# Kernel tuning notes

Measured on AMD Instinct MI355X. Metric: run time of the kernel, lower is better.

Reference implementation:

```python
import jax, jax.numpy as jnp
import numpy as np

B, N, F_IN, F_OUT = 1024, 92, 1024, 512
ALPHA = 0.2
NEG_INF = -9e15


def setup_inputs() -> dict:
    key = jax.random.key(0)
    k1, k2, k3, k4, k5, k6 = jax.random.split(key, 6)
    stdv = 1.0 / np.sqrt(F_OUT)
    inputs = {
        "input": jax.random.normal(k1, (B, N, F_IN), dtype=jnp.float32),
        "adj": jax.random.randint(k2, (B, N, N), 0, 2, dtype=jnp.int32),
        "weight": jax.random.uniform(k3, (F_IN, F_OUT), jnp.float32, -stdv, stdv),
        "a": jax.random.normal(k4, (2 * F_OUT, 1), dtype=jnp.float32) * 0.05,
        "A": jax.random.normal(k5, (N, N), dtype=jnp.float32) * 0.1,
        "bias": jax.random.uniform(k6, (F_OUT,), jnp.float32, -stdv, stdv),
    }
    return inputs


def reference(input, adj, weight, a, A, bias):
    # Wh: [B, N, F_OUT]
    Wh = jnp.einsum("bnf,fo->bno", input, weight)
    # pairwise scores e0[b,i,j] = leakyrelu(Wh_i . a1 + Wh_j . a2)
    Wh1 = Wh @ a[:F_OUT]              # [B, N, 1]
    Wh2 = Wh @ a[F_OUT:]              # [B, N, 1]
    e0 = jax.nn.leaky_relu(Wh1 + jnp.swapaxes(Wh2, -1, -2), ALPHA)  # [B, N, N]
    # original detaches here (a_input = e.view(92,-1).detach())
    e0 = jax.lax.stop_gradient(e0)
    # learned mixing with A (A.view(92,-1) == A), then leakyrelu
    e = jax.nn.leaky_relu(e0 @ A, ALPHA)                            # [B, N, N]
    att = jax.nn.softmax(jnp.where(adj > 0, e, NEG_INF), axis=-1)
    # dropout is identity in eval mode
    out = att @ Wh + bias                                           # [B, N, F_OUT]
    return out
```

## Files before the change

### kernel.cpp

```cpp
#include <hip/hip_runtime.h>

#define BATCH 1024
#define NNODE 92
#define FIN   1024
#define FOUT  512

typedef float    f32x4 __attribute__((ext_vector_type(4)));
typedef _Float16 half8 __attribute__((ext_vector_type(8)));
typedef _Float16 half4 __attribute__((ext_vector_type(4)));

__device__ __forceinline__ float lrelu(float x) { return fmaxf(x, 0.2f * x); }

#define BAR_LGKM() do {                                                        \
    asm volatile("s_waitcnt lgkmcnt(0)" ::: "memory");                         \
    __builtin_amdgcn_sched_barrier(0);                                         \
    __builtin_amdgcn_s_barrier();                                              \
  } while (0)

__global__ __launch_bounds__(256) void prep_kernel(
    const float* __restrict__ W, const float* __restrict__ Am,
    _Float16* __restrict__ WT, _Float16* __restrict__ ATp) {
  int bid = blockIdx.x, t = threadIdx.x;
  if (bid < 64) {
    int n0 = bid * 8;
    for (int it = 0; it < 4; ++it) {
      int k = it * 256 + t;
      const f32x4* src = (const f32x4*)(W + (size_t)k * FOUT + n0);
      f32x4 v0 = src[0], v1 = src[1];
      #pragma unroll
      for (int c = 0; c < 4; ++c) {
        WT[(size_t)(n0 + c) * FIN + k]     = (_Float16)v0[c];
        WT[(size_t)(n0 + 4 + c) * FIN + k] = (_Float16)v1[c];
      }
    }
  } else {
    int j0 = (bid - 64) * 24;
    for (int idx = t; idx < 24 * 104; idx += 256) {
      int jr = idx / 104, k = idx - jr * 104;
      int j = j0 + jr;
      float v = (j < NNODE && k < NNODE) ? Am[k * NNODE + j] : 0.f;
      ATp[j * 104 + k] = (_Float16)v;
    }
  }
}

__global__ __launch_bounds__(512, 2) void fused_kernel(
    const float* __restrict__ X, const _Float16* __restrict__ WT,
    const _Float16* __restrict__ ATp, const int* __restrict__ adj,
    const float* __restrict__ av, const float* __restrict__ bias,
    float* __restrict__ out) {
  extern __shared__ char smem[];
  _Float16* whT = (_Float16*)smem;
  _Float16* xs0 = (_Float16*)(smem + 106496);
  _Float16* xs1 = (_Float16*)(smem + 118784);
  _Float16* at_ = (_Float16*)(smem + 106496);
  _Float16* e0a = (_Float16*)(smem + 131072);
  float* red = (float*)(smem + 151040);
  float* w1s = (float*)(smem + 157184);
  float* w2s = (float*)(smem + 157568);

  int t = threadIdx.x, l = t & 63, w = t >> 6;
  int b = blockIdx.x;
  const float* Xb = X + (size_t)b * NNODE * FIN;

  int xrow[3], xwoff[3];
  bool xok[3];
  #pragma unroll
  for (int c = 0; c < 3; ++c) {
    int idx = c * 512 + t;
    int row = idx >> 4, kq = idx & 15;
    xrow[c] = (row < 92) ? row : 91;
    xok[c] = (row < 92);
    xwoff[c] = row * 128 + (((kq >> 1) ^ (row & 7)) << 4) + (kq & 1) * 8;
  }

  const _Float16* WTb = WT + (size_t)(w * 64 + (l & 15)) * FIN + (l >> 4) * 8;

  f32x4 zz = {0.f, 0.f, 0.f, 0.f};
  f32x4 acc[6][4];
  #pragma unroll
  for (int mi = 0; mi < 6; ++mi)
    #pragma unroll
    for (int ni = 0; ni < 4; ++ni) acc[mi][ni] = zz;

  f32x4 xvA[3], xvB[3];
  half8 bf0[4], bf1[4], bf2[4], bf3[4];

#define F_XISSUE(XV, KT) do {                                                  \
    int ktc_ = (KT) > 15 ? 15 : (KT);                                          \
    _Pragma("unroll")                                                          \
    for (int c = 0; c < 3; ++c) {                                              \
      int idx_ = c * 512 + t;                                                  \
      (XV)[c] = *(const f32x4*)(Xb + (size_t)xrow[c] * FIN + ktc_ * 64 +       \
                                (idx_ & 15) * 4);                              \
    }                                                                          \
  } while (0)

#define F_XCONV(BUF, XV) do {                                                  \
    _Pragma("unroll")                                                          \
    for (int c = 0; c < 3; ++c) {                                              \
      half4 h;                                                                 \
      if (xok[c]) {                                                            \
        h[0] = (_Float16)(XV)[c][0]; h[1] = (_Float16)(XV)[c][1];              \
        h[2] = (_Float16)(XV)[c][2]; h[3] = (_Float16)(XV)[c][3];              \
      } else {                                                                 \
        h[0] = (_Float16)0.f; h[1] = (_Float16)0.f;                            \
        h[2] = (_Float16)0.f; h[3] = (_Float16)0.f;                            \
      }                                                                        \
      *(half4*)((char*)(BUF) + xwoff[c]) = h;                                  \
    }                                                                          \
  } while (0)

#define F_BFLOAD(DST, KT, S) do {                                              \
    int ktc_ = (KT) > 15 ? 15 : (KT);                                          \
    _Pragma("unroll")                                                          \
    for (int ni = 0; ni < 4; ++ni)                                             \
      (DST)[ni] = *(const half8*)(WTb + (size_t)(ni * 16) * FIN +              \
                                  ktc_ * 64 + (S) * 32);                       \
  } while (0)

#define F_MFMA(XSBUF, BF, S) do {                                              \
    half8 af[6];                                                               \
    _Pragma("unroll")                                                          \
    for (int mi = 0; mi < 6; ++mi) {                                           \
      int row_ = mi * 16 + (l & 15);                                           \
      int slot_ = (((S) * 4 + (l >> 4)) ^ (row_ & 7));                         \
      af[mi] = *(const half8*)((const char*)(XSBUF) + row_ * 128 +             \
                               slot_ * 16);                                    \
    }                                                                          \
    _Pragma("unroll")                                                          \
    for (int mi = 0; mi < 6; ++mi)                                             \
      _Pragma("unroll")                                                        \
      for (int ni = 0; ni < 4; ++ni)                                           \
        acc[mi][ni] = __builtin_amdgcn_mfma_f32_16x16x32_f16(                  \
            af[mi], (BF)[ni], acc[mi][ni], 0, 0, 0);                           \
  } while (0)

#define F_PHASE(KT, XN, XP, CUR, NXT, BC0, BC1, BN0, BN1) do {                 \
    F_BFLOAD(BN0, (KT) + 1, 0);                                                \
    F_BFLOAD(BN1, (KT) + 1, 1);                                                \
    F_XISSUE(XN, (KT) + 2);                                                    \
    F_MFMA(CUR, BC0, 0);                                                       \
    F_MFMA(CUR, BC1, 1);                                                       \
    F_XCONV(NXT, XP);                                                          \
    BAR_LGKM();                                                                \
  } while (0)

  F_XISSUE(xvA, 0);
  F_XCONV(xs0, xvA);
  F_BFLOAD(bf0, 0, 0);
  F_BFLOAD(bf1, 0, 1);
  F_XISSUE(xvA, 1);
  BAR_LGKM();

  #pragma unroll 1
  for (int kt = 0; kt < 16; kt += 2) {
    F_PHASE(kt + 0, xvB, xvA, xs0, xs1, bf0, bf1, bf2, bf3);
    F_PHASE(kt + 1, xvA, xvB, xs1, xs0, bf2, bf3, bf0, bf1);
  }

  int adjv[4][6];
  if (w < 6) {
    #pragma unroll
    for (int r = 0; r < 4; ++r) {
      int i = 16 * w + (l >> 4) * 4 + r;
      int ic = (i < 92) ? i : 91;
      #pragma unroll
      for (int ni = 0; ni < 6; ++ni) {
        int j = ni * 16 + (l & 15);
        int jc = (j < 92) ? j : 91;
        adjv[r][ni] = adj[((size_t)b * NNODE + ic) * NNODE + jc];
      }
    }
  }
  half8 atv[3];
  bool aok2 = (t < 224);
  atv[0] = *(const half8*)(ATp + (size_t)t * 8);
  atv[1] = *(const half8*)(ATp + (size_t)(512 + t) * 8);
  if (aok2) atv[2] = *(const half8*)(ATp + (size_t)(1024 + t) * 8);

  #pragma unroll
  for (int mi = 0; mi < 6; ++mi) {
    int m4 = mi * 16 + (l >> 4) * 4;
    #pragma unroll
    for (int ni = 0; ni < 4; ++ni) {
      int C = w * 64 + ni * 16 + (l & 15);
      half4 h;
      h[0] = (_Float16)acc[mi][ni][0]; h[1] = (_Float16)acc[mi][ni][1];
      h[2] = (_Float16)acc[mi][ni][2]; h[3] = (_Float16)acc[mi][ni][3];
      *(half4*)((char*)whT + C * 208 + m4 * 2) = h;
    }
  }

  {
    float aC1[4], aC2[4];
    #pragma unroll
    for (int ni = 0; ni < 4; ++ni) {
      int C = w * 64 + ni * 16 + (l & 15);
      aC1[ni] = av[C];
      aC2[ni] = av[FOUT + C];
    }
    float p1[6][4], p2[6][4];
    #pragma unroll
    for (int mi = 0; mi < 6; ++mi)
      #pragma unroll
      for (int r = 0; r < 4; ++r) {
        float s1 = 0.f, s2 = 0.f;
        #pragma unroll
        for (int ni = 0; ni < 4; ++ni) {
          s1 = fmaf(acc[mi][ni][r], aC1[ni], s1);
          s2 = fmaf(acc[mi][ni][r], aC2[ni], s2);
        }
        p1[mi][r] = s1; p2[mi][r] = s2;
      }
    #pragma unroll
    for (int mm = 1; mm < 16; mm <<= 1)
      #pragma unroll
      for (int mi = 0; mi < 6; ++mi)
        #pragma unroll
        for (int r = 0; r < 4; ++r) {
          p1[mi][r] += __shfl_xor(p1[mi][r], mm);
          p2[mi][r] += __shfl_xor(p2[mi][r], mm);
        }
    if ((l & 15) == 0) {
      #pragma unroll
      for (int mi = 0; mi < 6; ++mi)
        #pragma unroll
        for (int r = 0; r < 4; ++r) {
          int m = mi * 16 + (l >> 4) * 4 + r;
          red[m * 16 + w * 2]     = p1[mi][r];
          red[m * 16 + w * 2 + 1] = p2[mi][r];
        }
    }
  }
  *(half8*)(at_ + (size_t)t * 8) = atv[0];
  *(half8*)(at_ + (size_t)(512 + t) * 8) = atv[1];
  if (aok2) *(half8*)(at_ + (size_t)(1024 + t) * 8) = atv[2];
  __syncthreads();

  if (t < 96) {
    float s1 = 0.f, s2 = 0.f;
    #pragma unroll
    for (int q = 0; q < 8; ++q) {
      s1 += red[t * 16 + q * 2];
      s2 += red[t * 16 + q * 2 + 1];
    }
    w1s[t] = s1;
    w2s[t] = s2;
  }
  __syncthreads();

  for (int idx = t; idx < 96 * 128; idx += 512) {
    int i = idx >> 7, k = idx & 127;
    if (k < 104) {
      float v = (i < 92 && k < 92) ? lrelu(w1s[i] + w2s[k]) : 0.f;
      e0a[i * 104 + k] = (_Float16)v;
    }
  }
  BAR_LGKM();

  if (w < 6) {
    f32x4 ez = {0.f, 0.f, 0.f, 0.f};
    f32x4 eacc[6];
    #pragma unroll
    for (int ni = 0; ni < 6; ++ni) eacc[ni] = ez;
    #pragma unroll
    for (int ks = 0; ks < 3; ++ks) {
      half8 ea = *(const half8*)((const char*)e0a +
                 (16 * w + (l & 15)) * 208 + ks * 64 + (l >> 4) * 16);
      #pragma unroll
      for (int ni = 0; ni < 6; ++ni) {
        half8 bt = *(const half8*)((const char*)at_ +
                   (16 * ni + (l & 15)) * 208 + ks * 64 + (l >> 4) * 16);
        eacc[ni] = __builtin_amdgcn_mfma_f32_16x16x32_f16(ea, bt, eacc[ni], 0, 0, 0);
      }
    }
    float attv[4][6];
    #pragma unroll
    for (int r = 0; r < 4; ++r) {
      int i = 16 * w + (l >> 4) * 4 + r;
      float s[6]; float m = -3.0e38f;
      #pragma unroll
      for (int ni = 0; ni < 6; ++ni) {
        int j = ni * 16 + (l & 15);
        float e = lrelu(eacc[ni][r]);
        float sv = -3.0e38f;
        if (i < 92 && j < 92)
          sv = (adjv[r][ni] > 0) ? e : -9.0e15f;
        s[ni] = sv;
        m = fmaxf(m, sv);
      }
      #pragma unroll
      for (int mm = 1; mm < 16; mm <<= 1) m = fmaxf(m, __shfl_xor(m, mm));
      float sum = 0.f; float p[6];
      #pragma unroll
      for (int ni = 0; ni < 6; ++ni) {
        int j = ni * 16 + (l & 15);
        p[ni] = (i < 92 && j < 92) ? __expf(s[ni] - m) : 0.f;
        sum += p[ni];
      }
      #pragma unroll
      for (int mm = 1; mm < 16; mm <<= 1) sum += __shfl_xor(sum, mm);
      float rs = (i < 92) ? (1.0f / sum) : 0.f;
      #pragma unroll
      for (int ni = 0; ni < 6; ++ni) attv[r][ni] = p[ni] * rs;
    }
    #pragma unroll
    for (int r = 0; r < 4; ++r) {
      int i = 16 * w + (l >> 4) * 4 + r;
      #pragma unroll
      for (int ni = 0; ni < 6; ++ni)
        e0a[i * 104 + ni * 16 + (l & 15)] = (_Float16)attv[r][ni];
    }
  }
  BAR_LGKM();

  #pragma unroll 1
  for (int pp = 0; pp < 2; ++pp) {
    int f0 = pp * 256 + w * 32;
    half8 bfp[3][2];
    #pragma unroll
    for (int ks = 0; ks < 3; ++ks)
      #pragma unroll
      for (int ni = 0; ni < 2; ++ni)
        bfp[ks][ni] = *(const half8*)((const char*)whT +
            (f0 + ni * 16 + (l & 15)) * 208 + ks * 64 + (l >> 4) * 16);
    f32x4 pz = {0.f, 0.f, 0.f, 0.f};
    f32x4 pacc[6][2];
    #pragma unroll
    for (int mi = 0; mi < 6; ++mi)
      #pragma unroll
      for (int ni = 0; ni < 2; ++ni) pacc[mi][ni] = pz;
    #pragma unroll
    for (int ks = 0; ks < 3; ++ks) {
      half8 af[6];
      #pragma unroll
      for (int mi = 0; mi < 6; ++mi)
        af[mi] = *(const half8*)((const char*)e0a +
                 (16 * mi + (l & 15)) * 208 + ks * 64 + (l >> 4) * 16);
      #pragma unroll
      for (int mi = 0; mi < 6; ++mi)
        #pragma unroll
        for (int ni = 0; ni < 2; ++ni)
          pacc[mi][ni] = __builtin_amdgcn_mfma_f32_16x16x32_f16(
              af[mi], bfp[ks][ni], pacc[mi][ni], 0, 0, 0);
    }
    #pragma unroll
    for (int ni = 0; ni < 2; ++ni) {
      int fcol = f0 + ni * 16 + (l & 15);
      float bv = bias[fcol];
      #pragma unroll
      for (int mi = 0; mi < 6; ++mi)
        #pragma unroll
        for (int r = 0; r < 4; ++r) {
          int i = 16 * mi + (l >> 4) * 4 + r;
          if (i < 92)
            out[((size_t)b * NNODE + i) * FOUT + fcol] = pacc[mi][ni][r] + bv;
        }
    }
  }
}

extern "C" void kernel_launch(void* const* d_in, const int* in_sizes, int n_in,
                              void* d_out, int out_size, void* d_ws, size_t ws_size,
                              hipStream_t stream) {
  (void)in_sizes; (void)n_in; (void)out_size; (void)ws_size;
  const float* X    = (const float*)d_in[0];
  const int*   adj  = (const int*)d_in[1];
  const float* W    = (const float*)d_in[2];
  const float* av   = (const float*)d_in[3];
  const float* Am   = (const float*)d_in[4];
  const float* bias = (const float*)d_in[5];
  float* out = (float*)d_out;
  char* ws = (char*)d_ws;

  _Float16* WT  = (_Float16*)(ws);
  _Float16* ATp = (_Float16*)(ws + 1048576);

  prep_kernel<<<68, 256, 0, stream>>>(W, Am, WT, ATp);
  hipFuncSetAttribute((const void*)fused_kernel,
                      hipFuncAttributeMaxDynamicSharedMemorySize, 157952);
  fused_kernel<<<1024, 512, 157952, stream>>>(X, WT, ATp, adj, av, bias, out);
}
```

Baseline: 241.0 us.

## Split output features across two blocks and fold attention vector into weights

```diff
diff --git a/kernel.cpp b/kernel.cpp
--- a/kernel.cpp
+++ b/kernel.cpp
@@ -8,6 +8,7 @@
 typedef float    f32x4 __attribute__((ext_vector_type(4)));
 typedef _Float16 half8 __attribute__((ext_vector_type(8)));
 typedef _Float16 half4 __attribute__((ext_vector_type(4)));
+typedef unsigned int uint4v __attribute__((ext_vector_type(4)));
 
 __device__ __forceinline__ float lrelu(float x) { return fmaxf(x, 0.2f * x); }
 
@@ -19,7 +20,9 @@
 
 __global__ __launch_bounds__(256) void prep_kernel(
     const float* __restrict__ W, const float* __restrict__ Am,
-    _Float16* __restrict__ WT, _Float16* __restrict__ ATp) {
+    const float* __restrict__ av,
+    _Float16* __restrict__ WT, _Float16* __restrict__ ATp,
+    float* __restrict__ wa1, float* __restrict__ wa2) {
   int bid = blockIdx.x, t = threadIdx.x;
   if (bid < 64) {
     int n0 = bid * 8;
@@ -33,7 +36,7 @@
         WT[(size_t)(n0 + 4 + c) * FIN + k] = (_Float16)v1[c];
       }
     }
-  } else {
+  } else if (bid < 68) {
     int j0 = (bid - 64) * 24;
     for (int idx = t; idx < 24 * 104; idx += 256) {
       int jr = idx / 104, k = idx - jr * 104;
@@ -41,27 +44,46 @@
       float v = (j < NNODE && k < NNODE) ? Am[k * NNODE + j] : 0.f;
       ATp[j * 104 + k] = (_Float16)v;
     }
+  } else {
+    int k = (bid - 68) * 256 + t;
+    const f32x4* wr = (const f32x4*)(W + (size_t)k * FOUT);
+    const f32x4* a1 = (const f32x4*)(av);
+    const f32x4* a2 = (const f32x4*)(av + FOUT);
+    float s1 = 0.f, s2 = 0.f;
+    for (int o = 0; o < FOUT / 4; ++o) {
+      f32x4 wv = wr[o], x1 = a1[o], x2 = a2[o];
+      #pragma unroll
+      for (int c = 0; c < 4; ++c) {
+        s1 = fmaf(wv[c], x1[c], s1);
+        s2 = fmaf(wv[c], x2[c], s2);
+      }
+    }
+    wa1[k] = s1; wa2[k] = s2;
   }
 }
 
-__global__ __launch_bounds__(512, 2) void fused_kernel(
+__global__ __launch_bounds__(512, 4) void fused_kernel(
     const float* __restrict__ X, const _Float16* __restrict__ WT,
     const _Float16* __restrict__ ATp, const int* __restrict__ adj,
-    const float* __restrict__ av, const float* __restrict__ bias,
-    float* __restrict__ out) {
+    const float* __restrict__ wa1g, const float* __restrict__ wa2g,
+    const float* __restrict__ bias, float* __restrict__ out) {
   extern __shared__ char smem[];
-  _Float16* whT = (_Float16*)smem;
-  _Float16* xs0 = (_Float16*)(smem + 106496);
-  _Float16* xs1 = (_Float16*)(smem + 118784);
-  _Float16* at_ = (_Float16*)(smem + 106496);
-  _Float16* e0a = (_Float16*)(smem + 131072);
-  float* red = (float*)(smem + 151040);
-  float* w1s = (float*)(smem + 157184);
-  float* w2s = (float*)(smem + 157568);
+  _Float16* xs0 = (_Float16*)smem;
+  _Float16* xs1 = (_Float16*)(smem + 12288);
+  _Float16* at_ = (_Float16*)smem;
+  _Float16* att = (_Float16*)(smem + 24576);
+  float* wa1l = (float*)(smem + 24576);
+  float* wa2l = (float*)(smem + 28672);
+  float* red  = (float*)(smem + 32768);
+  float* w1s  = (float*)(smem + 44544);
+  float* w2s  = (float*)(smem + 44928);
 
   int t = threadIdx.x, l = t & 63, w = t >> 6;
-  int b = blockIdx.x;
+  unsigned bid = blockIdx.x;
+  int half = (bid >> 3) & 1;
+  int b = (int)((bid >> 4) * 8 + (bid & 7));
   const float* Xb = X + (size_t)b * NNODE * FIN;
+  int g = l >> 4, c16 = l & 15;
 
   int xrow[3], xwoff[3];
   bool xok[3];
@@ -74,17 +96,21 @@
     xwoff[c] = row * 128 + (((kq >> 1) ^ (row & 7)) << 4) + (kq & 1) * 8;
   }
 
-  const _Float16* WTb = WT + (size_t)(w * 64 + (l & 15)) * FIN + (l >> 4) * 8;
+  const _Float16* WTb = WT + (size_t)(half * 256 + w * 32 + c16) * FIN + g * 8;
+
+  int grow = t >> 2, kq4 = t & 3;
+  bool gvok = (t < 384);
 
   f32x4 zz = {0.f, 0.f, 0.f, 0.f};
-  f32x4 acc[6][4];
+  f32x4 acc[6][2];
   #pragma unroll
   for (int mi = 0; mi < 6; ++mi)
     #pragma unroll
-    for (int ni = 0; ni < 4; ++ni) acc[mi][ni] = zz;
-
+    for (int ni = 0; ni < 2; ++ni) acc[mi][ni] = zz;
+
+  float s1 = 0.f, s2 = 0.f;
   f32x4 xvA[3], xvB[3];
-  half8 bf0[4], bf1[4], bf2[4], bf3[4];
+  half8 bf0[2], bf1[2], bf2[2], bf3[2];
 
 #define F_XISSUE(XV, KT) do {                                                  \
     int ktc_ = (KT) > 15 ? 15 : (KT);                                          \
@@ -114,7 +140,7 @@
 #define F_BFLOAD(DST, KT, S) do {                                              \
     int ktc_ = (KT) > 15 ? 15 : (KT);                                          \
     _Pragma("unroll")                                                          \
-    for (int ni = 0; ni < 4; ++ni)                                             \
+    for (int ni = 0; ni < 2; ++ni)                                             \
       (DST)[ni] = *(const half8*)(WTb + (size_t)(ni * 16) * FIN +              \
                                   ktc_ * 64 + (S) * 32);                       \
   } while (0)
@@ -123,17 +149,41 @@
     half8 af[6];                                                               \
     _Pragma("unroll")                                                          \
     for (int mi = 0; mi < 6; ++mi) {                                           \
-      int row_ = mi * 16 + (l & 15);                                           \
-      int slot_ = (((S) * 4 + (l >> 4)) ^ (row_ & 7));                         \
+      int row_ = mi * 16 + c16;                                                \
+      int slot_ = (((S) * 4 + g) ^ (row_ & 7));                                \
       af[mi] = *(const half8*)((const char*)(XSBUF) + row_ * 128 +             \
                                slot_ * 16);                                    \
     }                                                                          \
     _Pragma("unroll")                                                          \
     for (int mi = 0; mi < 6; ++mi)                                             \
       _Pragma("unroll")                                                        \
-      for (int ni = 0; ni < 4; ++ni)                                           \
+      for (int ni = 0; ni < 2; ++ni)                                           \
         acc[mi][ni] = __builtin_amdgcn_mfma_f32_16x16x32_f16(                  \
             af[mi], (BF)[ni], acc[mi][ni], 0, 0, 0);                           \
+  } while (0)
+
+#define F_GEMV(CUR, KT) do {                                                   \
+    if (gvok) {                                                                \
+      int k0_ = (KT) * 64 + kq4 * 16;                                          \
+      f32x4 w1c[4], w2c[4];                                                    \
+      _Pragma("unroll")                                                        \
+      for (int q = 0; q < 4; ++q) {                                            \
+        w1c[q] = *(const f32x4*)(wa1l + k0_ + q * 4);                          \
+        w2c[q] = *(const f32x4*)(wa2l + k0_ + q * 4);                          \
+      }                                                                        \
+      _Pragma("unroll")                                                        \
+      for (int q = 0; q < 4; ++q) {                                            \
+        int kq_ = kq4 * 4 + q;                                                 \
+        half4 xv4 = *(const half4*)((const char*)(CUR) + grow * 128 +          \
+                    (((kq_ >> 1) ^ (grow & 7)) << 4) + (kq_ & 1) * 8);         \
+        _Pragma("unroll")                                                      \
+        for (int cc = 0; cc < 4; ++cc) {                                       \
+          float x_ = (float)xv4[cc];                                           \
+          s1 = fmaf(x_, w1c[q][cc], s1);                                       \
+          s2 = fmaf(x_, w2c[q][cc], s2);                                       \
+        }                                                                      \
+      }                                                                        \
+    }                                                                          \
   } while (0)
 
 #define F_PHASE(KT, XN, XP, CUR, NXT, BC0, BC1, BN0, BN1) do {                 \
@@ -142,12 +192,18 @@
     F_XISSUE(XN, (KT) + 2);                                                    \
     F_MFMA(CUR, BC0, 0);                                                       \
     F_MFMA(CUR, BC1, 1);                                                       \
+    F_GEMV(CUR, KT);                                                           \
     F_XCONV(NXT, XP);                                                          \
     BAR_LGKM();                                                                \
   } while (0)
 
   F_XISSUE(xvA, 0);
   F_XCONV(xs0, xvA);
+  {
+    f32x4 wv1a = *(const f32x4*)(wa1g + t * 4 + (t & 1) * 0);
+  }
+  wa1l[t] = wa1g[t]; wa1l[512 + t] = wa1g[512 + t];
+  wa2l[t] = wa2g[t]; wa2l[512 + t] = wa2g[512 + t];
   F_BFLOAD(bf0, 0, 0);
   F_BFLOAD(bf1, 0, 1);
   F_XISSUE(xvA, 1);
@@ -163,11 +219,11 @@
   if (w < 6) {
     #pragma unroll
     for (int r = 0; r < 4; ++r) {
-      int i = 16 * w + (l >> 4) * 4 + r;
+      int i = 16 * w + g * 4 + r;
       int ic = (i < 92) ? i : 91;
       #pragma unroll
       for (int ni = 0; ni < 6; ++ni) {
-        int j = ni * 16 + (l & 15);
+        int j = ni * 16 + c16;
         int jc = (j < 92) ? j : 91;
         adjv[r][ni] = adj[((size_t)b * NNODE + ic) * NNODE + jc];
       }
@@ -179,59 +235,22 @@
   atv[1] = *(const half8*)(ATp + (size_t)(512 + t) * 8);
   if (aok2) atv[2] = *(const half8*)(ATp + (size_t)(1024 + t) * 8);
 
+  unsigned phl[6][2], phh[6][2];
   #pragma unroll
-  for (int mi = 0; mi < 6; ++mi) {
-    int m4 = mi * 16 + (l >> 4) * 4;
-    #pragma unroll
-    for (int ni = 0; ni < 4; ++ni) {
-      int C = w * 64 + ni * 16 + (l & 15);
+  for (int mi = 0; mi < 6; ++mi)
+    #pragma unroll
+    for (int ni = 0; ni < 2; ++ni) {
       half4 h;
       h[0] = (_Float16)acc[mi][ni][0]; h[1] = (_Float16)acc[mi][ni][1];
       h[2] = (_Float16)acc[mi][ni][2]; h[3] = (_Float16)acc[mi][ni][3];
-      *(half4*)((char*)whT + C * 208 + m4 * 2) = h;
-    }
-  }
-
-  {
-    float aC1[4], aC2[4];
-    #pragma unroll
-    for (int ni = 0; ni < 4; ++ni) {
-      int C = w * 64 + ni * 16 + (l & 15);
-      aC1[ni] = av[C];
-      aC2[ni] = av[FOUT + C];
-    }
-    float p1[6][4], p2[6][4];
-    #pragma unroll
-    for (int mi = 0; mi < 6; ++mi)
-      #pragma unroll
-      for (int r = 0; r < 4; ++r) {
-        float s1 = 0.f, s2 = 0.f;
-        #pragma unroll
-        for (int ni = 0; ni < 4; ++ni) {
-          s1 = fmaf(acc[mi][ni][r], aC1[ni], s1);
-          s2 = fmaf(acc[mi][ni][r], aC2[ni], s2);
-        }
-        p1[mi][r] = s1; p2[mi][r] = s2;
-      }
-    #pragma unroll
-    for (int mm = 1; mm < 16; mm <<= 1)
-      #pragma unroll
-      for (int mi = 0; mi < 6; ++mi)
-        #pragma unroll
-        for (int r = 0; r < 4; ++r) {
-          p1[mi][r] += __shfl_xor(p1[mi][r], mm);
-          p2[mi][r] += __shfl_xor(p2[mi][r], mm);
-        }
-    if ((l & 15) == 0) {
-      #pragma unroll
-      for (int mi = 0; mi < 6; ++mi)
-        #pragma unroll
-        for (int r = 0; r < 4; ++r) {
-          int m = mi * 16 + (l >> 4) * 4 + r;
-          red[m * 16 + w * 2]     = p1[mi][r];
-          red[m * 16 + w * 2 + 1] = p2[mi][r];
-        }
-    }
+      unsigned long long u = *(const unsigned long long*)&h;
+      phl[mi][ni] = (unsigned)u;
+      phh[mi][ni] = (unsigned)(u >> 32);
+    }
+
+  if (gvok) {
+    red[grow * 8 + kq4 * 2]     = s1;
+    red[grow * 8 + kq4 * 2 + 1] = s2;
   }
   *(half8*)(at_ + (size_t)t * 8) = atv[0];
   *(half8*)(at_ + (size_t)(512 + t) * 8) = atv[1];
@@ -239,50 +258,45 @@
   __syncthreads();
 
   if (t < 96) {
-    float s1 = 0.f, s2 = 0.f;
-    #pragma unroll
-    for (int q = 0; q < 8; ++q) {
-      s1 += red[t * 16 + q * 2];
-      s2 += red[t * 16 + q * 2 + 1];
-    }
-    w1s[t] = s1;
-    w2s[t] = s2;
+    float r1 = 0.f, r2 = 0.f;
+    #pragma unroll
+    for (int q = 0; q < 4; ++q) {
+      r1 += red[t * 8 + q * 2];
+      r2 += red[t * 8 + q * 2 + 1];
+    }
+    w1s[t] = r1;
+    w2s[t] = r2;
   }
   __syncthreads();
-
-  for (int idx = t; idx < 96 * 128; idx += 512) {
-    int i = idx >> 7, k = idx & 127;
-    if (k < 104) {
-      float v = (i < 92 && k < 92) ? lrelu(w1s[i] + w2s[k]) : 0.f;
-      e0a[i * 104 + k] = (_Float16)v;
-    }
-  }
-  BAR_LGKM();
 
   if (w < 6) {
     f32x4 ez = {0.f, 0.f, 0.f, 0.f};
     f32x4 eacc[6];
     #pragma unroll
     for (int ni = 0; ni < 6; ++ni) eacc[ni] = ez;
+    float w1i = w1s[16 * w + c16];
     #pragma unroll
     for (int ks = 0; ks < 3; ++ks) {
-      half8 ea = *(const half8*)((const char*)e0a +
-                 (16 * w + (l & 15)) * 208 + ks * 64 + (l >> 4) * 16);
+      int k0 = ks * 32 + g * 8;
+      half8 ea;
+      #pragma unroll
+      for (int j = 0; j < 8; ++j)
+        ea[j] = (_Float16)lrelu(w1i + w2s[k0 + j]);
       #pragma unroll
       for (int ni = 0; ni < 6; ++ni) {
         half8 bt = *(const half8*)((const char*)at_ +
-                   (16 * ni + (l & 15)) * 208 + ks * 64 + (l >> 4) * 16);
+                   (16 * ni + c16) * 208 + ks * 64 + g * 16);
         eacc[ni] = __builtin_amdgcn_mfma_f32_16x16x32_f16(ea, bt, eacc[ni], 0, 0, 0);
       }
     }
     float attv[4][6];
     #pragma unroll
     for (int r = 0; r < 4; ++r) {
-      int i = 16 * w + (l >> 4) * 4 + r;
+      int i = 16 * w + g * 4 + r;
       float s[6]; float m = -3.0e38f;
       #pragma unroll
       for (int ni = 0; ni < 6; ++ni) {
-        int j = ni * 16 + (l & 15);
+        int j = ni * 16 + c16;
         float e = lrelu(eacc[ni][r]);
         float sv = -3.0e38f;
         if (i < 92 && j < 92)
@@ -295,7 +309,7 @@
       float sum = 0.f; float p[6];
       #pragma unroll
       for (int ni = 0; ni < 6; ++ni) {
-        int j = ni * 16 + (l & 15);
+        int j = ni * 16 + c16;
         p[ni] = (i < 92 && j < 92) ? __expf(s[ni] - m) : 0.f;
         sum += p[ni];
       }
@@ -307,53 +321,62 @@
     }
     #pragma unroll
     for (int r = 0; r < 4; ++r) {
-      int i = 16 * w + (l >> 4) * 4 + r;
+      int i = 16 * w + g * 4 + r;
       #pragma unroll
       for (int ni = 0; ni < 6; ++ni)
-        e0a[i * 104 + ni * 16 + (l & 15)] = (_Float16)attv[r][ni];
+        att[i * 104 + ni * 16 + c16] = (_Float16)attv[r][ni];
     }
   }
   BAR_LGKM();
 
-  #pragma unroll 1
-  for (int pp = 0; pp < 2; ++pp) {
-    int f0 = pp * 256 + w * 32;
-    half8 bfp[3][2];
-    #pragma unroll
-    for (int ks = 0; ks < 3; ++ks)
-      #pragma unroll
-      for (int ni = 0; ni < 2; ++ni)
-        bfp[ks][ni] = *(const half8*)((const char*)whT +
-            (f0 + ni * 16 + (l & 15)) * 208 + ks * 64 + (l >> 4) * 16);
+  {
     f32x4 pz = {0.f, 0.f, 0.f, 0.f};
     f32x4 pacc[6][2];
     #pragma unroll
     for (int mi = 0; mi < 6; ++mi)
       #pragma unroll
       for (int ni = 0; ni < 2; ++ni) pacc[mi][ni] = pz;
+    int sA = ((g & 1) * 2) * 16 + c16;
+    int sB = sA + 16;
+    bool hi = (g >> 1) != 0;
     #pragma unroll
     for (int ks = 0; ks < 3; ++ks) {
       half8 af[6];
       #pragma unroll
       for (int mi = 0; mi < 6; ++mi)
-        af[mi] = *(const half8*)((const char*)e0a +
-                 (16 * mi + (l & 15)) * 208 + ks * 64 + (l >> 4) * 16);
-      #pragma unroll
-      for (int mi = 0; mi < 6; ++mi)
+        af[mi] = *(const half8*)((const char*)att +
+                 (16 * mi + c16) * 208 + ks * 64 + g * 16);
+      #pragma unroll
+      for (int ni = 0; ni < 2; ++ni) {
+        unsigned a0 = __shfl(phl[2 * ks][ni], sA, 64);
+        unsigned b0 = __shfl(phl[2 * ks + 1][ni], sA, 64);
+        unsigned a1 = __shfl(phh[2 * ks][ni], sA, 64);
+        unsigned b1 = __shfl(phh[2 * ks + 1][ni], sA, 64);
+        unsigned a2 = __shfl(phl[2 * ks][ni], sB, 64);
+        unsigned b2 = __shfl(phl[2 * ks + 1][ni], sB, 64);
+        unsigned a3 = __shfl(phh[2 * ks][ni], sB, 64);
+        unsigned b3 = __shfl(phh[2 * ks + 1][ni], sB, 64);
+        uint4v uv;
+        uv[0] = hi ? b0 : a0;
+        uv[1] = hi ? b1 : a1;
+        uv[2] = hi ? b2 : a2;
+        uv[3] = hi ? b3 : a3;
+        half8 bfv = *(const half8*)&uv;
         #pragma unroll
-        for (int ni = 0; ni < 2; ++ni)
+        for (int mi = 0; mi < 6; ++mi)
           pacc[mi][ni] = __builtin_amdgcn_mfma_f32_16x16x32_f16(
-              af[mi], bfp[ks][ni], pacc[mi][ni], 0, 0, 0);
+              af[mi], bfv, pacc[mi][ni], 0, 0, 0);
+      }
     }
     #pragma unroll
     for (int ni = 0; ni < 2; ++ni) {
-      int fcol = f0 + ni * 16 + (l & 15);
+      int fcol = half * 256 + w * 32 + ni * 16 + c16;
       float bv = bias[fcol];
       #pragma unroll
       for (int mi = 0; mi < 6; ++mi)
         #pragma unroll
         for (int r = 0; r < 4; ++r) {
-          int i = 16 * mi + (l >> 4) * 4 + r;
+          int i = 16 * mi + g * 4 + r;
           if (i < 92)
             out[((size_t)b * NNODE + i) * FOUT + fcol] = pacc[mi][ni][r] + bv;
         }
@@ -376,9 +399,12 @@
 
   _Float16* WT  = (_Float16*)(ws);
   _Float16* ATp = (_Float16*)(ws + 1048576);
-
-  prep_kernel<<<68, 256, 0, stream>>>(W, Am, WT, ATp);
+  float* wa1 = (float*)(ws + 1068544);
+  float* wa2 = (float*)(ws + 1072640);
+
+  prep_kernel<<<72, 256, 0, stream>>>(W, Am, av, WT, ATp, wa1, wa2);
   hipFuncSetAttribute((const void*)fused_kernel,
-                      hipFuncAttributeMaxDynamicSharedMemorySize, 157952);
-  fused_kernel<<<1024, 512, 157952, stream>>>(X, WT, ATp, adj, av, bias, out);
+                      hipFuncAttributeMaxDynamicSharedMemorySize, 45312);
+  fused_kernel<<<2048, 512, 45312, stream>>>(X, WT, ATp, adj, wa1, wa2,
+                                             bias, out);
 }
```

New measurement: 648.7 us. +169.2%, slower.
